# Kernel optimization log

Hardware: AMD Instinct MI355X
Metric: run time of the kernel (lower is better)

Reference implementation:

```python
import jax, jax.numpy as jnp
import numpy as np
from jax import lax

N, E = 10000, 100000
IN_CH, HID, EDGE_DIM, K = 32, 64, 16, 3
DILATIONS = (1, 2, 4)


def setup_inputs() -> dict:
    key = jax.random.key(0)
    ks = jax.random.split(key, 20)
    def nrm(k, shape, fan):
        return jax.random.normal(k, shape, jnp.float32) * (1.0 / np.sqrt(fan))
    inp = {
        "x": jax.random.normal(ks[0], (N, IN_CH), jnp.float32),
        "edge_attr": jax.random.normal(ks[1], (E, EDGE_DIM), jnp.float32),
        "h_prev": jax.random.normal(ks[2], (N, K, HID), jnp.float32),
        "edge_index": jax.random.randint(ks[3], (2, E), 0, N, jnp.int32),
        # edge-conditioning MLP: edge_dim -> 32 -> in_ch*hid
        "w1": nrm(ks[4], (EDGE_DIM, 32), EDGE_DIM), "b1": jnp.zeros((32,), jnp.float32),
        "w2": nrm(ks[5], (32, IN_CH * HID), 32), "b2": jnp.zeros((IN_CH * HID,), jnp.float32),
        # NNConv root weight + bias
        "root": nrm(ks[6], (IN_CH, HID), IN_CH), "bias": jnp.zeros((HID,), jnp.float32),
        # three dilated Conv1d layers [out, in, k]
        "tcn_w1": nrm(ks[7], (HID, HID, K), HID * K), "tcn_b1": jnp.zeros((HID,), jnp.float32),
        "tcn_w2": nrm(ks[8], (HID, HID, K), HID * K), "tcn_b2": jnp.zeros((HID,), jnp.float32),
        "tcn_w3": nrm(ks[9], (HID, HID, K), HID * K), "tcn_b3": jnp.zeros((HID,), jnp.float32),
        # output projection hid*3 -> hid
        "proj_w": nrm(ks[10], (HID * len(DILATIONS), HID), HID * len(DILATIONS)),
        "proj_b": jnp.zeros((HID,), jnp.float32),
    }
    return inp


def _conv1d_last(h, w, b, dilation):
    # h: [N, C, L], w: [O, I, K]; 'same'-style padding (K-1)*d//2, return last timestep.
    pad = (K - 1) * dilation // 2
    out = lax.conv_general_dilated(
        h, w, window_strides=(1,), padding=[(pad, pad)],
        rhs_dilation=(dilation,), dimension_numbers=("NCH", "OIH", "NCH"))
    return out[:, :, -1] + b[None, :]


def reference(x, edge_attr, h_prev, edge_index,
              w1, b1, w2, b2, root, bias,
              tcn_w1, tcn_b1, tcn_w2, tcn_b2, tcn_w3, tcn_b3,
              proj_w, proj_b):
    src, dst = edge_index[0], edge_index[1]
    n = x.shape[0]

    # --- NNConv (ECC): per-edge weight via MLP, gather -> matmul -> scatter-mean ---
    h_e = jax.nn.relu(edge_attr @ w1 + b1)                   # [E, 32]
    W_e = (h_e @ w2 + b2).reshape(-1, IN_CH, HID)            # [E, in, hid]
    msg = jnp.einsum("ei,eio->eo", x[src], W_e)             # [E, hid]
    agg = jax.ops.segment_sum(msg, dst, num_segments=n)      # [N, hid]
    cnt = jax.ops.segment_sum(jnp.ones((msg.shape[0],), msg.dtype), dst, num_segments=n)
    mean = agg / jnp.maximum(cnt, 1.0)[:, None]
    h_graph = jax.nn.relu(mean + x @ root + bias)            # [N, hid]

    # --- history update ---
    h_hist = jnp.concatenate([h_prev[:, 1:], h_graph[:, None, :]], axis=1)  # [N, K, hid]

    # --- dilated TCN stack, keep only last timestep of each branch ---
    h_in = jnp.transpose(h_hist, (0, 2, 1))                  # [N, hid, K]
    outs = [
        _conv1d_last(h_in, tcn_w1, tcn_b1, DILATIONS[0]),
        _conv1d_last(h_in, tcn_w2, tcn_b2, DILATIONS[1]),
        _conv1d_last(h_in, tcn_w3, tcn_b3, DILATIONS[2]),
    ]
    h_cat = jnp.concatenate(outs, axis=1)                    # [N, hid*3]
    h_out = h_cat @ proj_w + proj_b                          # dropout = identity (eval)
    return h_out, h_hist
```

## Files before the change

kernel.cpp:

```cpp
#include <hip/hip_runtime.h>
#include <stdint.h>

#define NN 10000
#define NE 100000
#define CHUNK 10

__device__ __forceinline__ float bu2f(uint16_t u) {
    return __uint_as_float(((uint32_t)u) << 16);
}
__device__ __forceinline__ float blo(uint32_t v) { return __uint_as_float(v << 16); }
__device__ __forceinline__ float bhi(uint32_t v) { return __uint_as_float(v & 0xffff0000u); }
__device__ __forceinline__ uint16_t f2bu(float f) {
    uint32_t u = __float_as_uint(f);
    return (uint16_t)((u + 0x7fffu + ((u >> 16) & 1u)) >> 16);
}
__device__ __forceinline__ float ldf(const void* p, size_t i, int f32) {
    return f32 ? ((const float*)p)[i] : bu2f(((const uint16_t*)p)[i]);
}
struct f8 { float v[8]; };
__device__ __forceinline__ f8 ldf8(const void* p, size_t i, int f32) {
    f8 r;
    if (f32) {
        const float4* q = (const float4*)((const float*)p + i);
        float4 a = q[0], b = q[1];
        r.v[0]=a.x; r.v[1]=a.y; r.v[2]=a.z; r.v[3]=a.w;
        r.v[4]=b.x; r.v[5]=b.y; r.v[6]=b.z; r.v[7]=b.w;
    } else {
        uint4 u = *(const uint4*)((const uint16_t*)p + i);
        r.v[0]=blo(u.x); r.v[1]=bhi(u.x); r.v[2]=blo(u.y); r.v[3]=bhi(u.y);
        r.v[4]=blo(u.z); r.v[5]=bhi(u.z); r.v[6]=blo(u.w); r.v[7]=bhi(u.w);
    }
    return r;
}
__device__ __forceinline__ void stf(void* p, size_t i, float v, int f32) {
    if (f32) ((float*)p)[i] = v;
    else ((uint16_t*)p)[i] = f2bu(v);
}
__device__ __forceinline__ int clampi(int v, int lo, int hi) {
    return min(max(v, lo), hi);
}

__global__ __launch_bounds__(256) void k_init(
    const void* __restrict__ x, float4* __restrict__ zbase, int* __restrict__ flag)
{
    __shared__ int red[256];
    int bid = blockIdx.x;
    int tid = threadIdx.x;
    if (bid < 657) {
        int idx = bid * 256 + tid;
        if (idx < 168088) zbase[idx] = make_float4(0.f, 0.f, 0.f, 0.f);
    } else {
        const uint16_t* p = (const uint16_t*)x;
        int c = 0;
        #pragma unroll
        for (int q = 0; q < 4; q++) {
            float a = fabsf(bu2f(p[tid + q * 256]));
            if (a > 1e-3f && a < 16.0f) c++;
        }
        red[tid] = c;
        __syncthreads();
        #pragma unroll
        for (int d = 128; d > 0; d >>= 1) {
            if (tid < d) red[tid] += red[tid + d];
            __syncthreads();
        }
        if (tid == 0) *flag = (red[0] < 870) ? 1 : 0;
    }
}

__global__ __launch_bounds__(256, 4) void k_prep(
    const void* __restrict__ x, const void* __restrict__ root,
    const void* __restrict__ tw1, const void* __restrict__ tw2,
    const void* __restrict__ tw3,
    const void* __restrict__ tb1, const void* __restrict__ tb2,
    const void* __restrict__ tb3,
    const void* __restrict__ proj_w,
    const void* __restrict__ edge_attr, const void* __restrict__ w1,
    const void* __restrict__ b1,
    const void* __restrict__ w2, const void* __restrict__ b2,
    const int* __restrict__ ei, const int* __restrict__ flag,
    float* __restrict__ xs_f, float* __restrict__ root_f,
    float* __restrict__ A, float* __restrict__ B, float* __restrict__ C,
    float* __restrict__ dv,
    int* __restrict__ outdeg, int* __restrict__ indeg, int* __restrict__ rank,
    uint16_t* __restrict__ h_edge,
    uint16_t* __restrict__ T, float* __restrict__ xb)
{
    int bid = blockIdx.x;
    int tid = threadIdx.x;
    __shared__ union PU {
        struct { float xs[8][32]; uint16_t Ts[32][64]; } t;
        struct { float w1s[512]; float b1s[32]; float eas[32][16]; } mlp;
    } su;

    if (bid < 1250) {
        int f32 = *flag;
        int n0 = bid * 8;
        if (tid < 32) {
            f8 r = ldf8(x, (size_t)n0 * 32 + (size_t)tid * 8, f32);
            int base = tid * 8;
            #pragma unroll
            for (int q = 0; q < 8; q++) su.t.xs[(base + q) >> 5][(base + q) & 31] = r.v[q];
        }
        __syncthreads();
        int j = tid >> 3;
        int o0 = (tid & 7) * 8;
        float acc[8][8];
        #pragma unroll
        for (int s = 0; s < 8; s++)
            #pragma unroll
            for (int r = 0; r < 8; r++) acc[s][r] = 0.0f;
        if (f32) {
            const float* wb = (const float*)w2 + (size_t)j * 2048 + o0;
            for (int i = 0; i < 32; i++) {
                float4 a4 = *(const float4*)(wb + i * 64);
                float4 b4 = *(const float4*)(wb + i * 64 + 4);
                #pragma unroll
                for (int s = 0; s < 8; s++) {
                    float xv = su.t.xs[s][i];
                    acc[s][0] = fmaf(xv, a4.x, acc[s][0]); acc[s][1] = fmaf(xv, a4.y, acc[s][1]);
                    acc[s][2] = fmaf(xv, a4.z, acc[s][2]); acc[s][3] = fmaf(xv, a4.w, acc[s][3]);
                    acc[s][4] = fmaf(xv, b4.x, acc[s][4]); acc[s][5] = fmaf(xv, b4.y, acc[s][5]);
                    acc[s][6] = fmaf(xv, b4.z, acc[s][6]); acc[s][7] = fmaf(xv, b4.w, acc[s][7]);
                }
            }
        } else {
            const uint16_t* wb = (const uint16_t*)w2 + (size_t)j * 2048 + o0;
            for (int i = 0; i < 32; i++) {
                uint4 u = *(const uint4*)(wb + i * 64);
                float w0 = blo(u.x), w1_ = bhi(u.x), w2_ = blo(u.y), w3 = bhi(u.y);
                float w4 = blo(u.z), w5 = bhi(u.z), w6 = blo(u.w), w7 = bhi(u.w);
                #pragma unroll
                for (int s = 0; s < 8; s++) {
                    float xv = su.t.xs[s][i];
                    acc[s][0] = fmaf(xv, w0, acc[s][0]); acc[s][1] = fmaf(xv, w1_, acc[s][1]);
                    acc[s][2] = fmaf(xv, w2_, acc[s][2]); acc[s][3] = fmaf(xv, w3, acc[s][3]);
                    acc[s][4] = fmaf(xv, w4, acc[s][4]); acc[s][5] = fmaf(xv, w5, acc[s][5]);
                    acc[s][6] = fmaf(xv, w6, acc[s][6]); acc[s][7] = fmaf(xv, w7, acc[s][7]);
                }
            }
        }
        int k = tid >> 6, o = tid & 63;
        #pragma unroll
        for (int s = 0; s < 8; s++) {
            uint4 ov;
            ov.x = ((uint32_t)f2bu(acc[s][1]) << 16) | f2bu(acc[s][0]);
            ov.y = ((uint32_t)f2bu(acc[s][3]) << 16) | f2bu(acc[s][2]);
            ov.z = ((uint32_t)f2bu(acc[s][5]) << 16) | f2bu(acc[s][4]);
            ov.w = ((uint32_t)f2bu(acc[s][7]) << 16) | f2bu(acc[s][6]);
            *(uint4*)&su.t.Ts[j][o0] = ov;
            __syncthreads();
            uint16_t v0 = su.t.Ts[k * 8 + 0][o];
            uint16_t v1 = su.t.Ts[k * 8 + 1][o];
            uint16_t v2 = su.t.Ts[k * 8 + 2][o];
            uint16_t v3 = su.t.Ts[k * 8 + 3][o];
            uint16_t v4 = su.t.Ts[k * 8 + 4][o];
            uint16_t v5 = su.t.Ts[k * 8 + 5][o];
            uint16_t v6 = su.t.Ts[k * 8 + 6][o];
            uint16_t v7 = su.t.Ts[k * 8 + 7][o];
            uint4 tv_;
            tv_.x = (uint32_t)v0 | ((uint32_t)v1 << 16);
            tv_.y = (uint32_t)v2 | ((uint32_t)v3 << 16);
            tv_.z = (uint32_t)v4 | ((uint32_t)v5 << 16);
            tv_.w = (uint32_t)v6 | ((uint32_t)v7 << 16);
            *(uint4*)(T + (size_t)(n0 + s) * 2048 + (size_t)o * 32 + k * 8) = tv_;
            __syncthreads();
        }
        {
            int oo = tid & 63;
            if (f32) {
                const float* b2f = (const float*)b2;
                #pragma unroll
                for (int h = 0; h < 2; h++) {
                    int s = (tid >> 6) + h * 4;
                    float a2 = 0.0f;
                    #pragma unroll
                    for (int i = 0; i < 32; i++)
                        a2 = fmaf(su.t.xs[s][i], b2f[i * 64 + oo], a2);
                    xb[(size_t)(n0 + s) * 64 + oo] = a2;
                }
            } else {
                const uint16_t* b2u = (const uint16_t*)b2;
                #pragma unroll
                for (int h = 0; h < 2; h++) {
                    int s = (tid >> 6) + h * 4;
                    float a2 = 0.0f;
                    #pragma unroll
                    for (int i = 0; i < 32; i++)
                        a2 = fmaf(su.t.xs[s][i], bu2f(b2u[i * 64 + oo]), a2);
                    xb[(size_t)(n0 + s) * 64 + oo] = a2;
                }
            }
        }
    } else if (bid < 4375) {
        int f32 = *flag;
        int e0 = (bid - 1250) * 32;
        if (tid < 64) {
            f8 r = ldf8(w1, (size_t)tid * 8, f32);
            #pragma unroll
            for (int q = 0; q < 8; q++) su.mlp.w1s[tid * 8 + q] = r.v[q];
        } else if (tid < 128) {
            int t = tid - 64;
            f8 r = ldf8(edge_attr, (size_t)e0 * 16 + (size_t)t * 8, f32);
            int el = t >> 1, half = (t & 1) * 8;
            #pragma unroll
            for (int q = 0; q < 8; q++) su.mlp.eas[el][half + q] = r.v[q];
        } else if (tid < 160) {
            su.mlp.b1s[tid - 128] = ldf(b1, tid - 128, f32);
        }
        __syncthreads();
        int el = tid >> 5, jj = tid & 31;
        float wreg[16];
        #pragma unroll
        for (int k = 0; k < 16; k++) wreg[k] = su.mlp.w1s[k * 32 + jj];
        float bj = su.mlp.b1s[jj];
        #pragma unroll
        for (int r = 0; r < 4; r++) {
            int e = el + r * 8;
            float acc = bj;
            #pragma unroll
            for (int k = 0; k < 16; k++) acc = fmaf(su.mlp.eas[e][k], wreg[k], acc);
            h_edge[(size_t)(e0 + e) * 32 + jj] = f2bu(fmaxf(acc, 0.0f));
        }
    } else if (bid < 4887) {
        int f32 = *flag;
        int beta = bid - 4375;
        int i = beta >> 3;
        int chunk = beta & 7;
        int o = tid & 63, sub = tid >> 6;
        int cc0 = chunk * 8 + sub * 2;
        float a = 0.f, b = 0.f, c = 0.f, d = 0.f;
        #pragma unroll
        for (int m = 0; m < 2; m++) {
            int cc = cc0 + m;
            float p0 = ldf(proj_w, (size_t)cc * 64 + o, f32);
            float p1 = ldf(proj_w, (size_t)(64 + cc) * 64 + o, f32);
            float p2 = ldf(proj_w, (size_t)(128 + cc) * 64 + o, f32);
            size_t base = (size_t)cc * 192 + i * 3;
            a = fmaf(ldf(tw1, base + 1, f32), p0, a);
            a = fmaf(ldf(tw2, base + 1, f32), p1, a);
            a = fmaf(ldf(tw3, base + 1, f32), p2, a);
            b = fmaf(ldf(tw2, base + 0, f32), p1, b);
            c = fmaf(ldf(tw1, base + 0, f32), p0, c);
            if (i == 0) {
                d = fmaf(ldf(tb1, cc, f32), p0, d);
                d = fmaf(ldf(tb2, cc, f32), p1, d);
                d = fmaf(ldf(tb3, cc, f32), p2, d);
            }
        }
        unsafeAtomicAdd(&A[i * 64 + o], a);
        unsafeAtomicAdd(&B[i * 64 + o], b);
        unsafeAtomicAdd(&C[i * 64 + o], c);
        if (i == 0) unsafeAtomicAdd(&dv[o], d);
    } else if (bid < 5278) {
        int e = (bid - 4887) * 256 + tid;
        if (e < NE) {
            int src = clampi(ei[e], 0, NN - 1);
            rank[e] = atomicAdd(&outdeg[src], 1);
            atomicAdd(&indeg[clampi(ei[NE + e], 0, NN - 1)], 1);
        }
    } else if (bid < 5435) {
        int f32 = *flag;
        int v8 = (bid - 5278) * 256 + tid;
        if (v8 < 40000) {
            f8 r = ldf8(x, (size_t)v8 * 8, f32);
            float4* o = (float4*)(xs_f + (size_t)v8 * 8);
            o[0] = make_float4(r.v[0], r.v[1], r.v[2], r.v[3]);
            o[1] = make_float4(r.v[4], r.v[5], r.v[6], r.v[7]);
        }
    } else {
        int f32 = *flag;
        f8 r = ldf8(root, (size_t)tid * 8, f32);
        float4* o = (float4*)(root_f + (size_t)tid * 8);
        o[0] = make_float4(r.v[0], r.v[1], r.v[2], r.v[3]);
        o[1] = make_float4(r.v[4], r.v[5], r.v[6], r.v[7]);
    }
}

__global__ __launch_bounds__(256) void k_scat(
    const int* __restrict__ ei, const int* __restrict__ outdeg,
    const int* __restrict__ rank,
    int* __restrict__ sorted_src, int* __restrict__ sorted_dst,
    int* __restrict__ sorted_eid,
    const uint16_t* __restrict__ h_edge, uint16_t* __restrict__ h_srt, int hs_mode)
{
    __shared__ int offs_l[NN];
    __shared__ int tsum[256];
    int tid = threadIdx.x;
    const int CH = 40;
    int base = tid * CH;
    int s = 0;
    for (int k = 0; k < CH; k++) {
        int i = base + k;
        if (i < NN) s += outdeg[i];
    }
    tsum[tid] = s;
    __syncthreads();
    for (int d = 1; d < 256; d <<= 1) {
        int t = (tid >= d) ? tsum[tid - d] : 0;
        __syncthreads();
        if (tid >= d) tsum[tid] += t;
        __syncthreads();
    }
    int run = (tid == 0) ? 0 : tsum[tid - 1];
    for (int k = 0; k < CH; k++) {
        int i = base + k;
        if (i < NN) { offs_l[i] = run; run += outdeg[i]; }
    }
    __syncthreads();
    #pragma unroll
    for (int r = 0; r < 4; r++) {
        int e = blockIdx.x * 1024 + r * 256 + tid;
        if (e < NE) {
            int src = clampi(ei[e], 0, NN - 1);
            int dst = clampi(ei[NE + e], 0, NN - 1);
            int pos = clampi(offs_l[src] + rank[e], 0, NE - 1);
            sorted_src[pos] = src;
            sorted_dst[pos] = dst;
            if (hs_mode) {
                const uint4* hs = (const uint4*)(h_edge + (size_t)e * 32);
                uint4* hd = (uint4*)(h_srt + (size_t)pos * 32);
                hd[0] = hs[0]; hd[1] = hs[1]; hd[2] = hs[2]; hd[3] = hs[3];
            } else {
                sorted_eid[pos] = e;
            }
        }
    }
}

__global__ __launch_bounds__(256) void k_msg_g(
    const uint16_t* __restrict__ h_edge, const uint16_t* __restrict__ h_srt,
    int hs_mode, const uint16_t* __restrict__ T,
    const float* __restrict__ xb, const int* __restrict__ sorted_src,
    const int* __restrict__ sorted_dst, const int* __restrict__ sorted_eid,
    float* __restrict__ agg)
{
    int wid = blockIdx.x * 4 + (threadIdx.x >> 6);
    int lane = threadIdx.x & 63;
    int p0 = wid * CHUNK;
    if (p0 >= NE) return;
    int p1 = min(p0 + CHUNK, NE);
    int cur = -1;
    float tv[32];
    float xbv = 0.0f;
    int sN = clampi(sorted_src[p0], 0, NN - 1);
    const uint4* hq;
    if (hs_mode) hq = (const uint4*)(h_srt + (size_t)p0 * 32);
    else hq = (const uint4*)(h_edge + (size_t)clampi(sorted_eid[p0], 0, NE - 1) * 32);
    uint4 na = hq[0], nb = hq[1], nc = hq[2], nd = hq[3];
    const uint4* Tq = (const uint4*)(T + (size_t)sN * 2048 + (size_t)lane * 32);
    uint4 Tr0 = Tq[0], Tr1 = Tq[1], Tr2 = Tq[2], Tr3 = Tq[3];
    float xbN = xb[(size_t)sN * 64 + lane];
    for (int p = p0; p < p1; p++) {
        int s = sN;
        uint4 a = na, b = nb, c = nc, d = nd;
        if (s != cur) {
            cur = s;
            tv[0]=blo(Tr0.x); tv[1]=bhi(Tr0.x); tv[2]=blo(Tr0.y); tv[3]=bhi(Tr0.y);
            tv[4]=blo(Tr0.z); tv[5]=bhi(Tr0.z); tv[6]=blo(Tr0.w); tv[7]=bhi(Tr0.w);
            tv[8]=blo(Tr1.x); tv[9]=bhi(Tr1.x); tv[10]=blo(Tr1.y); tv[11]=bhi(Tr1.y);
            tv[12]=blo(Tr1.z); tv[13]=bhi(Tr1.z); tv[14]=blo(Tr1.w); tv[15]=bhi(Tr1.w);
            tv[16]=blo(Tr2.x); tv[17]=bhi(Tr2.x); tv[18]=blo(Tr2.y); tv[19]=bhi(Tr2.y);
            tv[20]=blo(Tr2.z); tv[21]=bhi(Tr2.z); tv[22]=blo(Tr2.w); tv[23]=bhi(Tr2.w);
            tv[24]=blo(Tr3.x); tv[25]=bhi(Tr3.x); tv[26]=blo(Tr3.y); tv[27]=bhi(Tr3.y);
            tv[28]=blo(Tr3.z); tv[29]=bhi(Tr3.z); tv[30]=blo(Tr3.w); tv[31]=bhi(Tr3.w);
            xbv = xbN;
        }
        int dst = clampi(sorted_dst[p], 0, NN - 1);
        if (p + 1 < p1) {
            sN = clampi(sorted_src[p + 1], 0, NN - 1);
            const uint4* h2;
            if (hs_mode) h2 = (const uint4*)(h_srt + (size_t)(p + 1) * 32);
            else h2 = (const uint4*)(h_edge + (size_t)clampi(sorted_eid[p + 1], 0, NE - 1) * 32);
            na = h2[0]; nb = h2[1]; nc = h2[2]; nd = h2[3];
            if (sN != cur) {
                const uint4* T2q = (const uint4*)(T + (size_t)sN * 2048 + (size_t)lane * 32);
                Tr0 = T2q[0]; Tr1 = T2q[1]; Tr2 = T2q[2]; Tr3 = T2q[3];
                xbN = xb[(size_t)sN * 64 + lane];
            }
        }
        float s0 = 0.f, s1 = 0.f, s2 = 0.f, s3 = 0.f;
        s0 = fmaf(blo(a.x), tv[0],  s0); s0 = fmaf(bhi(a.x), tv[1],  s0);
        s0 = fmaf(blo(a.y), tv[2],  s0); s0 = fmaf(bhi(a.y), tv[3],  s0);
        s0 = fmaf(blo(a.z), tv[4],  s0); s0 = fmaf(bhi(a.z), tv[5],  s0);
        s0 = fmaf(blo(a.w), tv[6],  s0); s0 = fmaf(bhi(a.w), tv[7],  s0);
        s1 = fmaf(blo(b.x), tv[8],  s1); s1 = fmaf(bhi(b.x), tv[9],  s1);
        s1 = fmaf(blo(b.y), tv[10], s1); s1 = fmaf(bhi(b.y), tv[11], s1);
        s1 = fmaf(blo(b.z), tv[12], s1); s1 = fmaf(bhi(b.z), tv[13], s1);
        s1 = fmaf(blo(b.w), tv[14], s1); s1 = fmaf(bhi(b.w), tv[15], s1);
        s2 = fmaf(blo(c.x), tv[16], s2); s2 = fmaf(bhi(c.x), tv[17], s2);
        s2 = fmaf(blo(c.y), tv[18], s2); s2 = fmaf(bhi(c.y), tv[19], s2);
        s2 = fmaf(blo(c.z), tv[20], s2); s2 = fmaf(bhi(c.z), tv[21], s2);
        s2 = fmaf(blo(c.w), tv[22], s2); s2 = fmaf(bhi(c.w), tv[23], s2);
        s3 = fmaf(blo(d.x), tv[24], s3); s3 = fmaf(bhi(d.x), tv[25], s3);
        s3 = fmaf(blo(d.y), tv[26], s3); s3 = fmaf(bhi(d.y), tv[27], s3);
        s3 = fmaf(blo(d.z), tv[28], s3); s3 = fmaf(bhi(d.z), tv[29], s3);
        s3 = fmaf(blo(d.w), tv[30], s3); s3 = fmaf(bhi(d.w), tv[31], s3);
        float acc = xbv + (s0 + s1) + (s2 + s3);
        unsafeAtomicAdd(&agg[(size_t)dst * 64 + lane], acc);
    }
}

__global__ __launch_bounds__(256) void k_node_out(
    const float* __restrict__ agg, const int* __restrict__ indeg,
    const float* __restrict__ xs_f, const float* __restrict__ root_f,
    const void* __restrict__ bias, const void* __restrict__ h_prev,
    const float* __restrict__ A, const float* __restrict__ B,
    const float* __restrict__ C, const float* __restrict__ dv,
    const void* __restrict__ proj_b,
    const int* __restrict__ flag, void* __restrict__ out)
{
    int f32 = *flag;
    int tid = threadIdx.x;
    int s = tid >> 6, o = tid & 63;
    int n = blockIdx.x * 4 + s;
    const size_t O1 = (size_t)NN * 64;
    __shared__ float hg_s[4][64], hp1_s[4][64], hp2_s[4][64];

    float xr = 0.0f;
    const float* xp = xs_f + (size_t)n * 32;
    #pragma unroll
    for (int i = 0; i < 32; i++)
        xr = fmaf(xp[i], root_f[i * 64 + o], xr);
    float c = (float)indeg[n];
    float m = agg[(size_t)n * 64 + o] / fmaxf(c, 1.0f);
    float hg = fmaxf(m + xr + ldf(bias, o, f32), 0.0f);
    float hp1 = ldf(h_prev, (size_t)n * 192 + 64 + o, f32);
    float hp2 = ldf(h_prev, (size_t)n * 192 + 128 + o, f32);
    hg_s[s][o] = hg; hp1_s[s][o] = hp1; hp2_s[s][o] = hp2;
    stf(out, O1 + (size_t)n * 192 + o, hp1, f32);
    stf(out, O1 + (size_t)n * 192 + 64 + o, hp2, f32);
    stf(out, O1 + (size_t)n * 192 + 128 + o, hg, f32);
    __syncthreads();

    float accA = 0.f, accB = 0.f, accC = 0.f;
    #pragma unroll 8
    for (int i = 0; i < 64; i++) {
        accA = fmaf(hg_s[s][i],  A[i * 64 + o], accA);
        accB = fmaf(hp1_s[s][i], B[i * 64 + o], accB);
        accC = fmaf(hp2_s[s][i], C[i * 64 + o], accC);
    }
    float acc = dv[o] + ldf(proj_b, o, f32) + (accA + accB) + accC;
    stf(out, (size_t)n * 64 + o, acc, f32);
}

static inline size_t align64(size_t v) { return (v + 63) & ~(size_t)63; }

extern "C" void kernel_launch(void* const* d_in, const int* in_sizes, int n_in,
                              void* d_out, int out_size, void* d_ws, size_t ws_size,
                              hipStream_t stream) {
    const void* x         = d_in[0];
    const void* edge_attr = d_in[1];
    const void* h_prev    = d_in[2];
    const int*  ei        = (const int*)d_in[3];
    const void* w1     = d_in[4];
    const void* b1     = d_in[5];
    const void* w2     = d_in[6];
    const void* b2     = d_in[7];
    const void* root   = d_in[8];
    const void* bias   = d_in[9];
    const void* tw1    = d_in[10];
    const void* tb1    = d_in[11];
    const void* tw2    = d_in[12];
    const void* tb2    = d_in[13];
    const void* tw3    = d_in[14];
    const void* tb3    = d_in[15];
    const void* proj_w = d_in[16];
    const void* proj_b = d_in[17];

    char* ws = (char*)d_ws;
    size_t off = 0;
    uint16_t* T      = (uint16_t*)(ws + off); off = align64(off + (size_t)NN * 2048 * 2);
    uint16_t* h_edge = (uint16_t*)(ws + off); off = align64(off + (size_t)NE * 32 * 2);
    float* xs_f   = (float*)(ws + off); off = align64(off + (size_t)NN * 32 * 4);
    float* root_f = (float*)(ws + off); off = align64(off + (size_t)2048 * 4);
    float* xb     = (float*)(ws + off); off = align64(off + (size_t)NN * 64 * 4);
    size_t zero_base = off;
    float* agg    = (float*)(ws + off); off = align64(off + (size_t)NN * 64 * 4);
    int* indeg    = (int*)(ws + off);   off = align64(off + (size_t)NN * 4);
    int* outdeg   = (int*)(ws + off);   off = align64(off + (size_t)NN * 4);
    float* Amat   = (float*)(ws + off); off = align64(off + (size_t)4096 * 4);
    float* Bmat   = (float*)(ws + off); off = align64(off + (size_t)4096 * 4);
    float* Cmat   = (float*)(ws + off); off = align64(off + (size_t)4096 * 4);
    float* dvec   = (float*)(ws + off); off = align64(off + (size_t)64 * 4);
    int* rank        = (int*)(ws + off); off = align64(off + (size_t)NE * 4);
    int* sorted_src  = (int*)(ws + off); off = align64(off + (size_t)NE * 4);
    int* sorted_dst  = (int*)(ws + off); off = align64(off + (size_t)NE * 4);
    int* sorted_eid  = (int*)(ws + off); off = align64(off + (size_t)NE * 4);
    int* flag        = (int*)(ws + off); off = align64(off + 64);
    uint16_t* h_srt  = (uint16_t*)(ws + off);
    size_t off_end = off + (size_t)NE * 32 * 2;
    int hs_mode = (off_end <= ws_size) ? 1 : 0;

    k_init<<<658, 256, 0, stream>>>(x, (float4*)((char*)d_ws + zero_base), flag);
    k_prep<<<5436, 256, 0, stream>>>(x, root, tw1, tw2, tw3, tb1, tb2, tb3,
                                     proj_w, edge_attr, w1, b1, w2, b2, ei, flag,
                                     xs_f, root_f, Amat, Bmat, Cmat, dvec,
                                     outdeg, indeg, rank, h_edge, T, xb);
    k_scat<<<(NE + 1023) / 1024, 256, 0, stream>>>(ei, outdeg, rank,
                                                   sorted_src, sorted_dst, sorted_eid,
                                                   h_edge, h_srt, hs_mode);
    k_msg_g<<<(NE / CHUNK + 3) / 4, 256, 0, stream>>>(h_edge, h_srt, hs_mode, T, xb,
                                                      sorted_src, sorted_dst,
                                                      sorted_eid, agg);
    k_node_out<<<NN / 4, 256, 0, stream>>>(agg, indeg, xs_f, root_f, bias, h_prev,
                                           Amat, Bmat, Cmat, dvec, proj_b, flag, d_out);
}
```

Before: 214.5 us.

## Hoist degree prefix scan into a separate single-block kernel before scatter

Moves the exclusive prefix scan over source out-degrees out of the scatter kernel, where every block recomputed it in shared memory, into a dedicated one-block 1024-thread scan kernel that writes offsets to global memory. The scatter kernel then processes one edge per thread across more blocks. This removes redundant per-block scanning and the large shared-memory footprint, at the cost of an extra kernel launch and a serial single-block stage.

```diff
diff --git a/kernel.cpp b/kernel.cpp
--- a/kernel.cpp
+++ b/kernel.cpp
@@ -277,53 +277,58 @@
     }
 }
 
+__global__ __launch_bounds__(1024) void k_scan(
+    const int* __restrict__ outdeg, int* __restrict__ offs)
+{
+    __shared__ int sums[1024];
+    const int CH = 10;
+    int tid = threadIdx.x;
+    int base = tid * CH;
+    int v[CH];
+    int s = 0;
+    #pragma unroll
+    for (int k = 0; k < CH; k++) {
+        int i = base + k;
+        int c = (i < NN) ? outdeg[i] : 0;
+        v[k] = s;
+        s += c;
+    }
+    sums[tid] = s;
+    __syncthreads();
+    for (int d = 1; d < 1024; d <<= 1) {
+        int t = (tid >= d) ? sums[tid - d] : 0;
+        __syncthreads();
+        if (tid >= d) sums[tid] += t;
+        __syncthreads();
+    }
+    int prefix = (tid == 0) ? 0 : sums[tid - 1];
+    #pragma unroll
+    for (int k = 0; k < CH; k++) {
+        int i = base + k;
+        if (i < NN) offs[i] = prefix + v[k];
+    }
+}
+
 __global__ __launch_bounds__(256) void k_scat(
-    const int* __restrict__ ei, const int* __restrict__ outdeg,
+    const int* __restrict__ ei, const int* __restrict__ offs,
     const int* __restrict__ rank,
     int* __restrict__ sorted_src, int* __restrict__ sorted_dst,
     int* __restrict__ sorted_eid,
     const uint16_t* __restrict__ h_edge, uint16_t* __restrict__ h_srt, int hs_mode)
 {
-    __shared__ int offs_l[NN];
-    __shared__ int tsum[256];
-    int tid = threadIdx.x;
-    const int CH = 40;
-    int base = tid * CH;
-    int s = 0;
-    for (int k = 0; k < CH; k++) {
-        int i = base + k;
-        if (i < NN) s += outdeg[i];
-    }
-    tsum[tid] = s;
-    __syncthreads();
-    for (int d = 1; d < 256; d <<= 1) {
-        int t = (tid >= d) ? tsum[tid - d] : 0;
-        __syncthreads();
-        if (tid >= d) tsum[tid] += t;
-        __syncthreads();
-    }
-    int run = (tid == 0) ? 0 : tsum[tid - 1];
-    for (int k = 0; k < CH; k++) {
-        int i = base + k;
-        if (i < NN) { offs_l[i] = run; run += outdeg[i]; }
-    }
-    __syncthreads();
-    #pragma unroll
-    for (int r = 0; r < 4; r++) {
-        int e = blockIdx.x * 1024 + r * 256 + tid;
-        if (e < NE) {
-            int src = clampi(ei[e], 0, NN - 1);
-            int dst = clampi(ei[NE + e], 0, NN - 1);
-            int pos = clampi(offs_l[src] + rank[e], 0, NE - 1);
-            sorted_src[pos] = src;
-            sorted_dst[pos] = dst;
-            if (hs_mode) {
-                const uint4* hs = (const uint4*)(h_edge + (size_t)e * 32);
-                uint4* hd = (uint4*)(h_srt + (size_t)pos * 32);
-                hd[0] = hs[0]; hd[1] = hs[1]; hd[2] = hs[2]; hd[3] = hs[3];
-            } else {
-                sorted_eid[pos] = e;
-            }
+    int e = blockIdx.x * 256 + threadIdx.x;
+    if (e < NE) {
+        int src = clampi(ei[e], 0, NN - 1);
+        int dst = clampi(ei[NE + e], 0, NN - 1);
+        int pos = clampi(offs[src] + rank[e], 0, NE - 1);
+        sorted_src[pos] = src;
+        sorted_dst[pos] = dst;
+        if (hs_mode) {
+            const uint4* hs = (const uint4*)(h_edge + (size_t)e * 32);
+            uint4* hd = (uint4*)(h_srt + (size_t)pos * 32);
+            hd[0] = hs[0]; hd[1] = hs[1]; hd[2] = hs[2]; hd[3] = hs[3];
+        } else {
+            sorted_eid[pos] = e;
         }
     }
 }
@@ -483,6 +488,7 @@
     float* Bmat   = (float*)(ws + off); off = align64(off + (size_t)4096 * 4);
     float* Cmat   = (float*)(ws + off); off = align64(off + (size_t)4096 * 4);
     float* dvec   = (float*)(ws + off); off = align64(off + (size_t)64 * 4);
+    int* offs        = (int*)(ws + off); off = align64(off + (size_t)(NN + 64) * 4);
     int* rank        = (int*)(ws + off); off = align64(off + (size_t)NE * 4);
     int* sorted_src  = (int*)(ws + off); off = align64(off + (size_t)NE * 4);
     int* sorted_dst  = (int*)(ws + off); off = align64(off + (size_t)NE * 4);
@@ -497,9 +503,10 @@
                                      proj_w, edge_attr, w1, b1, w2, b2, ei, flag,
                                      xs_f, root_f, Amat, Bmat, Cmat, dvec,
                                      outdeg, indeg, rank, h_edge, T, xb);
-    k_scat<<<(NE + 1023) / 1024, 256, 0, stream>>>(ei, outdeg, rank,
-                                                   sorted_src, sorted_dst, sorted_eid,
-                                                   h_edge, h_srt, hs_mode);
+    k_scan<<<1, 1024, 0, stream>>>(outdeg, offs);
+    k_scat<<<(NE + 255) / 256, 256, 0, stream>>>(ei, offs, rank,
+                                                 sorted_src, sorted_dst, sorted_eid,
+                                                 h_edge, h_srt, hs_mode);
     k_msg_g<<<(NE / CHUNK + 3) / 4, 256, 0, stream>>>(h_edge, h_srt, hs_mode, T, xb,
                                                       sorted_src, sorted_dst,
                                                       sorted_eid, agg);
```

Result: faster. 207.5 us (median of 3 runs) (-3.2%).
